# Kernel tuning notes

Measured on AMD Instinct MI355X. Metric: run time of the kernel, lower is better.

## Reference

```python
import jax, jax.numpy as jnp
import numpy as np
from jax import lax

B, OBS, E, H = 65536, 20, 64, 64


def setup_inputs() -> dict:
    key = jax.random.key(0)
    ks = jax.random.split(key, 13)
    s = 0.1
    inp = {
        "obs_traj": jax.random.normal(ks[0], (B, OBS, 2), jnp.float32),
        "W_emb": jax.random.normal(ks[1], (E, 2), jnp.float32) * s,
        "b_emb": jax.random.normal(ks[2], (E,), jnp.float32) * s,
        "Wih_e": jax.random.normal(ks[3], (4 * H, E), jnp.float32) * s,
        "Whh_e": jax.random.normal(ks[4], (4 * H, H), jnp.float32) * s,
        "bih_e": jax.random.normal(ks[5], (4 * H,), jnp.float32) * s,
        "bhh_e": jax.random.normal(ks[6], (4 * H,), jnp.float32) * s,
        "Wih_d": jax.random.normal(ks[7], (4 * H, E), jnp.float32) * s,
        "Whh_d": jax.random.normal(ks[8], (4 * H, H), jnp.float32) * s,
        "bih_d": jax.random.normal(ks[9], (4 * H,), jnp.float32) * s,
        "bhh_d": jax.random.normal(ks[10], (4 * H,), jnp.float32) * s,
        "W_fc": jax.random.normal(ks[11], (2, H), jnp.float32) * s,
        "b_fc": jax.random.normal(ks[12], (2,), jnp.float32) * s,
        "pred_len": 12,
    }
    return inp


def _lstm_step(x, h, c, Wih, Whh, b):
    # PyTorch LSTM gate order: i, f, g, o
    g = x @ Wih.T + h @ Whh.T + b  # [B, 4H]
    i, f, gg, o = jnp.split(g, 4, axis=-1)
    c2 = jax.nn.sigmoid(f) * c + jax.nn.sigmoid(i) * jnp.tanh(gg)
    h2 = jax.nn.sigmoid(o) * jnp.tanh(c2)
    return h2, c2


def reference(obs_traj, W_emb, b_emb, Wih_e, Whh_e, bih_e, bhh_e,
              Wih_d, Whh_d, bih_d, bhh_d, W_fc, b_fc, pred_len):
    bsz = obs_traj.shape[0]
    dt = obs_traj.dtype
    # Encoder: embed all observed steps at once, then scan the LSTM over time.
    emb = jax.nn.relu(obs_traj @ W_emb.T + b_emb)  # [B, OBS, E]
    b_e = bih_e + bhh_e
    h0 = jnp.zeros((bsz, H), dt)
    c0 = jnp.zeros((bsz, H), dt)

    def enc_step(carry, x_t):
        h, c = carry
        h, c = _lstm_step(x_t, h, c, Wih_e, Whh_e, b_e)
        return (h, c), None

    (h, c), _ = lax.scan(enc_step, (h0, c0), jnp.swapaxes(emb, 0, 1))

    b_d = bih_d + bhh_d
    dec_in = jax.nn.relu(obs_traj[:, -1, :] @ W_emb.T + b_emb)  # [B, E]

    def dec_step(carry, _):
        h, c, x = carry
        h, c = _lstm_step(x, h, c, Wih_d, Whh_d, b_d)
        pred = h @ W_fc.T + b_fc  # [B, 2]
        nxt = jax.nn.relu(pred @ W_emb.T + b_emb)
        return (h, c, nxt), pred

    _, preds = lax.scan(dec_step, (h, c, dec_in), None, length=pred_len)
    return jnp.swapaxes(preds, 0, 1)  # [B, pred_len, 2]
```

## Files before the change

### kernel.cpp

```cpp
#include <hip/hip_runtime.h>

typedef __bf16 bf16x8 __attribute__((ext_vector_type(8)));
typedef __bf16 bf16x4 __attribute__((ext_vector_type(4)));
typedef float  f32x4  __attribute__((ext_vector_type(4)));
typedef float  f32x2  __attribute__((ext_vector_type(2)));

constexpr int BATCH = 65536;
constexpr int OBS   = 20;
constexpr int PRED  = 12;
constexpr int BT    = 128;
constexpr int AST   = 136;

__device__ __forceinline__ float sigm(float x) {
    return __builtin_amdgcn_rcpf(1.0f + __builtin_amdgcn_exp2f(x * -1.4426950408889634f));
}
__device__ __forceinline__ float tanh_(float x) {
    return 1.0f - 2.0f * __builtin_amdgcn_rcpf(1.0f + __builtin_amdgcn_exp2f(x * 2.8853900817779268f));
}

struct SmallW {
    float  bcomb_e[256];
    float  bcomb_d[256];
    float4 embc[64];
    float  wfc[128];
    float  bfc[2];
};

__global__ __launch_bounds__(256, 2)
void vanilla_lstm(const float* __restrict__ obs,
                  const float* __restrict__ W_emb, const float* __restrict__ b_emb,
                  const float* __restrict__ Wih_e, const float* __restrict__ Whh_e,
                  const float* __restrict__ bih_e, const float* __restrict__ bhh_e,
                  const float* __restrict__ Wih_d, const float* __restrict__ Whh_d,
                  const float* __restrict__ bih_d, const float* __restrict__ bhh_d,
                  const float* __restrict__ W_fc,  const float* __restrict__ b_fc,
                  float* __restrict__ out)
{
    __shared__ __align__(16) __bf16 As[BT * AST];
    __shared__ __align__(16) float  pred_s[BT * 2];
    __shared__ SmallW sw;

    const int tid  = threadIdx.x;
    const int wv   = tid >> 6;
    const int lane = tid & 63;
    const int m    = lane & 15;
    const int q    = lane >> 4;
    const int wblk = wv * 16;
    const size_t gRow0 = (size_t)blockIdx.x * BT;

    sw.bcomb_e[tid] = bih_e[tid] + bhh_e[tid];
    sw.bcomb_d[tid] = bih_d[tid] + bhh_d[tid];
    if (tid < 64)  sw.embc[tid] = make_float4(W_emb[2 * tid], W_emb[2 * tid + 1], b_emb[tid], 0.f);
    if (tid < 128) sw.wfc[tid]  = W_fc[tid];
    if (tid < 2)   sw.bfc[tid]  = b_fc[tid];

    {
        uint4 z; z.x = z.y = z.z = z.w = 0u;
        uint4* p = (uint4*)As;
        constexpr int NV = BT * AST * 2 / 16;
        #pragma unroll
        for (int i = 0; i < NV / 256; ++i) p[tid + i * 256] = z;
        if (tid < (NV % 256)) p[tid + (NV / 256) * 256] = z;
    }

    bf16x8 bfr[4][4];
    auto load_bfr = [&](const float* Wih, const float* Whh) {
        #pragma unroll
        for (int c = 0; c < 4; ++c) {
            const int n = c * 64 + wblk + m;
            #pragma unroll
            for (int kt = 0; kt < 4; ++kt) {
                const float* s = (kt < 2) ? (Wih + n * 64 + kt * 32 + q * 8)
                                          : (Whh + n * 64 + (kt - 2) * 32 + q * 8);
                float4 a = *(const float4*)s;
                float4 b = *(const float4*)(s + 4);
                bf16x8 v;
                v[0] = (__bf16)a.x; v[1] = (__bf16)a.y; v[2] = (__bf16)a.z; v[3] = (__bf16)a.w;
                v[4] = (__bf16)b.x; v[5] = (__bf16)b.y; v[6] = (__bf16)b.z; v[7] = (__bf16)b.w;
                bfr[c][kt] = v;
            }
        }
    };
    load_bfr(Wih_e, Whh_e);

    f32x4 cst[8];
    #pragma unroll
    for (int i = 0; i < 8; ++i) cst[i] = f32x4{0.f, 0.f, 0.f, 0.f};

    __syncthreads();

    f32x4 bias4[4];
    auto load_bias = [&](const float* bc) {
        #pragma unroll
        for (int c = 0; c < 4; ++c)
            bias4[c] = *(const f32x4*)&bc[c * 64 + wblk + q * 4];
    };
    load_bias(sw.bcomb_e);

    f32x4 acc[4][4];

    auto gemm = [&](int chunk) {
        #pragma unroll
        for (int nt = 0; nt < 4; ++nt)
            #pragma unroll
            for (int c = 0; c < 4; ++c)
                acc[nt][c] = bias4[c];
        #pragma unroll
        for (int kt = 0; kt < 4; ++kt) {
            bf16x8 af[4];
            #pragma unroll
            for (int nt = 0; nt < 4; ++nt)
                af[nt] = *(const bf16x8*)&As[(chunk * 64 + nt * 16 + m) * AST + kt * 32 + q * 8];
            #pragma unroll
            for (int nt = 0; nt < 4; ++nt)
                #pragma unroll
                for (int c = 0; c < 4; ++c)
                    acc[nt][c] = __builtin_amdgcn_mfma_f32_16x16x32_bf16(
                        bfr[c][kt], af[nt], acc[nt][c], 0, 0, 0);
        }
    };

    auto update = [&](int chunk) {
        #pragma unroll
        for (int nt = 0; nt < 4; ++nt) {
            const int row = chunk * 64 + nt * 16 + m;
            f32x4 ci = cst[chunk * 4 + nt];
            bf16x4 h4;
            #pragma unroll
            for (int r = 0; r < 4; ++r) {
                const float cN = sigm(acc[nt][1][r]) * ci[r]
                               + sigm(acc[nt][0][r]) * tanh_(acc[nt][2][r]);
                ci[r] = cN;
                h4[r] = (__bf16)(sigm(acc[nt][3][r]) * tanh_(cN));
            }
            cst[chunk * 4 + nt] = ci;
            *(bf16x4*)&As[row * AST + 64 + wblk + q * 4] = h4;
        }
    };

    auto emb_row = [&](int row, float o0, float o1) {
        #pragma unroll
        for (int h8 = 0; h8 < 2; ++h8) {
            bf16x8 v;
            #pragma unroll
            for (int j = 0; j < 8; ++j) {
                float4 wc = sw.embc[wblk + h8 * 8 + j];
                v[j] = (__bf16)fmaxf(fmaf(o0, wc.x, fmaf(o1, wc.y, wc.z)), 0.f);
            }
            *(bf16x8*)&As[row * AST + wblk + h8 * 8] = v;
        }
    };

    const float* obr0 = obs + (gRow0 + lane) * (OBS * 2);
    const float* obr1 = obs + (gRow0 + 64 + lane) * (OBS * 2);

    {
        f32x2 o0 = *(const f32x2*)obr0;
        f32x2 o1 = *(const f32x2*)obr1;
        emb_row(lane, o0[0], o0[1]);
        emb_row(64 + lane, o1[0], o1[1]);
    }
    __syncthreads();
    gemm(0);

    for (int t = 0; t < OBS; ++t) {
        __syncthreads();
        f32x2 on0{0.f, 0.f};
        if (t + 1 < OBS) on0 = *(const f32x2*)(obr0 + (t + 1) * 2);
        update(0);
        gemm(1);
        if (t + 1 < OBS) emb_row(lane, on0[0], on0[1]);
        __syncthreads();
        f32x2 on1{0.f, 0.f};
        if (t + 1 < OBS) on1 = *(const f32x2*)(obr1 + (t + 1) * 2);
        update(1);
        if (t + 1 < OBS) {
            gemm(0);
            emb_row(64 + lane, on1[0], on1[1]);
        }
    }

    load_bfr(Wih_d, Whh_d);
    load_bias(sw.bcomb_d);
    gemm(0);

    auto pred_phase = [&](int chunk, int td) {
        const int prow = chunk * 64 + (tid >> 2);
        const int comp = (tid >> 1) & 1, half = tid & 1;
        const int cb = half * 32;
        float p = 0.f;
        #pragma unroll
        for (int e8 = 0; e8 < 4; ++e8) {
            bf16x8 hv = *(const bf16x8*)&As[prow * AST + 64 + cb + e8 * 8];
            f32x4 w0 = *(const f32x4*)&sw.wfc[comp * 64 + cb + e8 * 8];
            f32x4 w1 = *(const f32x4*)&sw.wfc[comp * 64 + cb + e8 * 8 + 4];
            p += (float)hv[0] * w0[0] + (float)hv[1] * w0[1] + (float)hv[2] * w0[2] + (float)hv[3] * w0[3]
               + (float)hv[4] * w1[0] + (float)hv[5] * w1[1] + (float)hv[6] * w1[2] + (float)hv[7] * w1[3];
        }
        p += __shfl_xor(p, 1, 64);
        if (half == 0) {
            p += sw.bfc[comp];
            pred_s[prow * 2 + comp] = p;
            out[((gRow0 + prow) * PRED + td) * 2 + comp] = p;
        }
    };
    auto emb_dec = [&](int chunk) {
        const int row = chunk * 64 + lane;
        f32x2 pv = *(const f32x2*)&pred_s[row * 2];
        emb_row(row, pv[0], pv[1]);
    };

    for (int td = 0; td < PRED; ++td) {
        __syncthreads();
        update(0);
        gemm(1);
        __syncthreads();
        update(1);
        pred_phase(0, td);
        __syncthreads();
        pred_phase(1, td);
        if (td + 1 < PRED) emb_dec(0);
        __syncthreads();
        if (td + 1 < PRED) {
            emb_dec(1);
            gemm(0);
        }
    }
}

extern "C" void kernel_launch(void* const* d_in, const int* in_sizes, int n_in,
                              void* d_out, int out_size, void* d_ws, size_t ws_size,
                              hipStream_t stream) {
    (void)in_sizes; (void)n_in; (void)d_ws; (void)ws_size; (void)out_size;
    const float* obs   = (const float*)d_in[0];
    const float* W_emb = (const float*)d_in[1];
    const float* b_emb = (const float*)d_in[2];
    const float* Wih_e = (const float*)d_in[3];
    const float* Whh_e = (const float*)d_in[4];
    const float* bih_e = (const float*)d_in[5];
    const float* bhh_e = (const float*)d_in[6];
    const float* Wih_d = (const float*)d_in[7];
    const float* Whh_d = (const float*)d_in[8];
    const float* bih_d = (const float*)d_in[9];
    const float* bhh_d = (const float*)d_in[10];
    const float* W_fc  = (const float*)d_in[11];
    const float* b_fc  = (const float*)d_in[12];
    float* o = (float*)d_out;

    dim3 grid(BATCH / BT), block(256);
    hipLaunchKernelGGL(vanilla_lstm, grid, block, 0, stream,
                       obs, W_emb, b_emb, Wih_e, Whh_e, bih_e, bhh_e,
                       Wih_d, Whh_d, bih_d, bhh_d, W_fc, b_fc, o);
}
```

Measured before the change: 307.4 us.

## Fold activation exp2 scaling into weights and interleave half-chunk GEMM with gate update

Pre-scales the LSTM weight fragments and biases by -log2(e) (or 2*log2(e) for the g gate) at load time, so the gate nonlinearities take exp2 directly without a multiply. The cell update is rewritten to merge sigmoid·tanh pairs into a single reciprocal each, cutting transcendental count. The per-chunk GEMM and update are split into halves and interleaved so MFMA work can overlap the VALU-heavy activation math. Pre-scaling before bf16 rounding slightly changes numerics, and exp2 arguments are clamped to avoid overflow.

```diff
diff --git a/kernel.cpp b/kernel.cpp
--- a/kernel.cpp
+++ b/kernel.cpp
@@ -11,12 +11,11 @@
 constexpr int BT    = 128;
 constexpr int AST   = 136;
 
-__device__ __forceinline__ float sigm(float x) {
-    return __builtin_amdgcn_rcpf(1.0f + __builtin_amdgcn_exp2f(x * -1.4426950408889634f));
-}
-__device__ __forceinline__ float tanh_(float x) {
-    return 1.0f - 2.0f * __builtin_amdgcn_rcpf(1.0f + __builtin_amdgcn_exp2f(x * 2.8853900817779268f));
-}
+constexpr float SIO = -1.4426950408889634f;
+constexpr float SG  =  2.8853900817779268f;
+
+__device__ __forceinline__ float exp2_(float x) { return __builtin_amdgcn_exp2f(x); }
+__device__ __forceinline__ float rcp_(float x)  { return __builtin_amdgcn_rcpf(x); }
 
 struct SmallW {
     float  bcomb_e[256];
@@ -67,6 +66,7 @@
     auto load_bfr = [&](const float* Wih, const float* Whh) {
         #pragma unroll
         for (int c = 0; c < 4; ++c) {
+            const float sc = (c == 2) ? SG : SIO;
             const int n = c * 64 + wblk + m;
             #pragma unroll
             for (int kt = 0; kt < 4; ++kt) {
@@ -75,8 +75,10 @@
                 float4 a = *(const float4*)s;
                 float4 b = *(const float4*)(s + 4);
                 bf16x8 v;
-                v[0] = (__bf16)a.x; v[1] = (__bf16)a.y; v[2] = (__bf16)a.z; v[3] = (__bf16)a.w;
-                v[4] = (__bf16)b.x; v[5] = (__bf16)b.y; v[6] = (__bf16)b.z; v[7] = (__bf16)b.w;
+                v[0] = (__bf16)(sc * a.x); v[1] = (__bf16)(sc * a.y);
+                v[2] = (__bf16)(sc * a.z); v[3] = (__bf16)(sc * a.w);
+                v[4] = (__bf16)(sc * b.x); v[5] = (__bf16)(sc * b.y);
+                v[6] = (__bf16)(sc * b.z); v[7] = (__bf16)(sc * b.w);
                 bfr[c][kt] = v;
             }
         }
@@ -92,48 +94,66 @@
     f32x4 bias4[4];
     auto load_bias = [&](const float* bc) {
         #pragma unroll
-        for (int c = 0; c < 4; ++c)
-            bias4[c] = *(const f32x4*)&bc[c * 64 + wblk + q * 4];
+        for (int c = 0; c < 4; ++c) {
+            const float sc = (c == 2) ? SG : SIO;
+            f32x4 b = *(const f32x4*)&bc[c * 64 + wblk + q * 4];
+            bias4[c] = f32x4{sc * b[0], sc * b[1], sc * b[2], sc * b[3]};
+        }
     };
     load_bias(sw.bcomb_e);
 
-    f32x4 acc[4][4];
-
-    auto gemm = [&](int chunk) {
-        #pragma unroll
-        for (int nt = 0; nt < 4; ++nt)
+    f32x4 acc[2][2][4];
+
+    auto gemm_sub = [&](int chunk, int half) {
+        #pragma unroll
+        for (int nt = 0; nt < 2; ++nt)
             #pragma unroll
             for (int c = 0; c < 4; ++c)
-                acc[nt][c] = bias4[c];
+                acc[half][nt][c] = bias4[c];
         #pragma unroll
         for (int kt = 0; kt < 4; ++kt) {
-            bf16x8 af[4];
-            #pragma unroll
-            for (int nt = 0; nt < 4; ++nt)
-                af[nt] = *(const bf16x8*)&As[(chunk * 64 + nt * 16 + m) * AST + kt * 32 + q * 8];
-            #pragma unroll
-            for (int nt = 0; nt < 4; ++nt)
+            bf16x8 af[2];
+            #pragma unroll
+            for (int nt = 0; nt < 2; ++nt)
+                af[nt] = *(const bf16x8*)&As[(chunk * 64 + (half * 2 + nt) * 16 + m) * AST + kt * 32 + q * 8];
+            #pragma unroll
+            for (int nt = 0; nt < 2; ++nt)
                 #pragma unroll
                 for (int c = 0; c < 4; ++c)
-                    acc[nt][c] = __builtin_amdgcn_mfma_f32_16x16x32_bf16(
-                        bfr[c][kt], af[nt], acc[nt][c], 0, 0, 0);
-        }
-    };
-
-    auto update = [&](int chunk) {
-        #pragma unroll
-        for (int nt = 0; nt < 4; ++nt) {
-            const int row = chunk * 64 + nt * 16 + m;
-            f32x4 ci = cst[chunk * 4 + nt];
+                    acc[half][nt][c] = __builtin_amdgcn_mfma_f32_16x16x32_bf16(
+                        bfr[c][kt], af[nt], acc[half][nt][c], 0, 0, 0);
+        }
+    };
+
+    auto update_sub = [&](int chunk, int half) {
+        #pragma unroll
+        for (int nt = 0; nt < 2; ++nt) {
+            const int idx = chunk * 4 + half * 2 + nt;
+            const int row = chunk * 64 + (half * 2 + nt) * 16 + m;
+            f32x4 ci = cst[idx];
             bf16x4 h4;
             #pragma unroll
             for (int r = 0; r < 4; ++r) {
-                const float cN = sigm(acc[nt][1][r]) * ci[r]
-                               + sigm(acc[nt][0][r]) * tanh_(acc[nt][2][r]);
+                const float gi = acc[half][nt][0][r];
+                const float gf = acc[half][nt][1][r];
+                const float gg = acc[half][nt][2][r];
+                const float go = acc[half][nt][3][r];
+                const float Ef = exp2_(gf);
+                const float a  = ci[r] * rcp_(1.0f + Ef);
+                const float Ei = exp2_(gi);
+                const float Eg = exp2_(fminf(fmaxf(gg, -80.f), 80.f));
+                const float d1 = 1.0f + Ei;
+                const float r1 = rcp_(fmaf(d1, Eg, d1));
+                const float cN = fmaf(Eg - 1.0f, r1, a);
+                const float Eo = exp2_(go);
+                const float Ec = exp2_(fminf(fmaxf(cN * SG, -80.f), 80.f));
+                const float d2 = 1.0f + Eo;
+                const float r2 = rcp_(fmaf(d2, Ec, d2));
+                const float h  = (Ec - 1.0f) * r2;
                 ci[r] = cN;
-                h4[r] = (__bf16)(sigm(acc[nt][3][r]) * tanh_(cN));
+                h4[r] = (__bf16)h;
             }
-            cst[chunk * 4 + nt] = ci;
+            cst[idx] = ci;
             *(bf16x4*)&As[row * AST + 64 + wblk + q * 4] = h4;
         }
     };
@@ -161,28 +181,34 @@
         emb_row(64 + lane, o1[0], o1[1]);
     }
     __syncthreads();
-    gemm(0);
+    gemm_sub(0, 0);
+    gemm_sub(0, 1);
 
     for (int t = 0; t < OBS; ++t) {
         __syncthreads();
         f32x2 on0{0.f, 0.f};
         if (t + 1 < OBS) on0 = *(const f32x2*)(obr0 + (t + 1) * 2);
-        update(0);
-        gemm(1);
+        update_sub(0, 0);
+        gemm_sub(1, 0);
+        update_sub(0, 1);
+        gemm_sub(1, 1);
         if (t + 1 < OBS) emb_row(lane, on0[0], on0[1]);
         __syncthreads();
         f32x2 on1{0.f, 0.f};
         if (t + 1 < OBS) on1 = *(const f32x2*)(obr1 + (t + 1) * 2);
-        update(1);
+        update_sub(1, 0);
+        if (t + 1 < OBS) gemm_sub(0, 0);
+        update_sub(1, 1);
         if (t + 1 < OBS) {
-            gemm(0);
+            gemm_sub(0, 1);
             emb_row(64 + lane, on1[0], on1[1]);
         }
     }
 
     load_bfr(Wih_d, Whh_d);
     load_bias(sw.bcomb_d);
-    gemm(0);
+    gemm_sub(0, 0);
+    gemm_sub(0, 1);
 
     auto pred_phase = [&](int chunk, int td) {
         const int prow = chunk * 64 + (tid >> 2);
@@ -212,10 +238,13 @@
 
     for (int td = 0; td < PRED; ++td) {
         __syncthreads();
-        update(0);
-        gemm(1);
-        __syncthreads();
-        update(1);
+        update_sub(0, 0);
+        gemm_sub(1, 0);
+        update_sub(0, 1);
+        gemm_sub(1, 1);
+        __syncthreads();
+        update_sub(1, 0);
+        update_sub(1, 1);
         pred_phase(0, td);
         __syncthreads();
         pred_phase(1, td);
@@ -223,7 +252,8 @@
         __syncthreads();
         if (td + 1 < PRED) {
             emb_dec(1);
-            gemm(0);
+            gemm_sub(0, 0);
+            gemm_sub(0, 1);
         }
     }
 }
```

Measured after the change: 285.2 us. -7.2%, faster.
